# Performance work log

Hardware: AMD Instinct MI355X
Metric: run time of the kernel (lower is better)

The kernel has to match this reference:

```python
import jax, jax.numpy as jnp
import numpy as np

N_NODES = 50000
N_EDGES = 800000
HIDDEN = 128
MAX_Z = 1000
NUM_GRAPHS = 1000
NODES_PER_GRAPH = N_NODES // NUM_GRAPHS


def setup_inputs() -> dict:
    key = jax.random.key(0)
    ks = jax.random.split(key, 12)
    s = 1.0 / np.sqrt(HIDDEN)
    inp = {
        "z": jax.random.randint(ks[0], (N_NODES,), 0, MAX_Z),
        "edge_index": jax.random.randint(ks[1], (2, N_EDGES), 0, N_NODES),
        # sorted batch ids, 50 nodes per graph (SEAL-style subgraph batch)
        "batch": jnp.repeat(jnp.arange(NUM_GRAPHS), NODES_PER_GRAPH),
        "num_graphs": NUM_GRAPHS,
        "emb_table": jax.random.normal(ks[2], (MAX_Z, HIDDEN), jnp.float32),
        "w0": jax.random.normal(ks[3], (HIDDEN, HIDDEN), jnp.float32) * s,
        "b0": jnp.zeros((HIDDEN,), jnp.float32),
        "w1": jax.random.normal(ks[4], (HIDDEN, HIDDEN), jnp.float32) * s,
        "b1": jnp.zeros((HIDDEN,), jnp.float32),
        "w2": jax.random.normal(ks[5], (HIDDEN, HIDDEN), jnp.float32) * s,
        "b2": jnp.zeros((HIDDEN,), jnp.float32),
        "lin1_w": jax.random.normal(ks[6], (HIDDEN, HIDDEN), jnp.float32) * s,
        "lin1_b": jnp.zeros((HIDDEN,), jnp.float32),
        "lin2_w": jax.random.normal(ks[7], (HIDDEN, 1), jnp.float32) * s,
        "lin2_b": jnp.zeros((1,), jnp.float32),
    }
    return inp


def reference(z, edge_index, batch, num_graphs, emb_table, w0, b0, w1, b1, w2, b2,
              lin1_w, lin1_b, lin2_w, lin2_b):
    n = z.shape[0]
    # GCN symmetric normalization with self-loops (PyG gcn_norm, edge_weight=1)
    loops = jnp.arange(n)
    src = jnp.concatenate([edge_index[0], loops])
    dst = jnp.concatenate([edge_index[1], loops])
    ones = jnp.ones(src.shape[0], dtype=emb_table.dtype)
    deg = jax.ops.segment_sum(ones, dst, num_segments=n)
    dinv = jnp.where(deg > 0, jax.lax.rsqrt(deg), 0.0)
    norm = dinv[src] * dinv[dst]  # [E+N]

    def gcn_conv(x, W, b):
        h = x @ W  # linear transform first (bias added after aggregation)
        msg = h[src] * norm[:, None]  # gather + scale over edges
        return jax.ops.segment_sum(msg, dst, num_segments=n) + b

    x = emb_table[z]  # z embedding (z is 1-D -> no sum over dim 1)
    # dropout is identity in eval mode
    x = jax.nn.relu(gcn_conv(x, w0, b0))
    x = jax.nn.relu(gcn_conv(x, w1, b1))
    x = gcn_conv(x, w2, b2)

    # first occurrence of each batch id (batch is sorted per PyG convention)
    center = jax.ops.segment_min(jnp.arange(n), batch, num_segments=num_graphs)
    g = x[center] * x[center + 1]  # [G, H] pairwise link readout
    g = jax.nn.relu(g @ lin1_w + lin1_b)
    return g @ lin2_w + lin2_b  # [G, 1]
```

## Files before the change

### kernel.cpp

```cpp
#include <hip/hip_runtime.h>
#include <hip/hip_fp16.h>
#include <cstdint>
#include <cstddef>

#define H 128

typedef _Float16 f16x8 __attribute__((ext_vector_type(8)));
typedef float f32x4 __attribute__((ext_vector_type(4)));

__device__ inline float2 up2(unsigned u) {
    return __half22float2(*reinterpret_cast<const __half2*>(&u));
}
__device__ inline unsigned pk2(float a, float b) {
    __half2 h = __floats2half2_rn(a, b);
    return *reinterpret_cast<unsigned*>(&h);
}

__global__ void init_kernel(int* __restrict__ fill, int n,
                            const float* __restrict__ w0, const float* __restrict__ w1,
                            const float* __restrict__ w2, _Float16* __restrict__ wt) {
    int idx = blockIdx.x * 256 + threadIdx.x;
    if (idx < n) fill[idx] = 0;
    if (idx < 3 * H * H) {
        int m = idx >> 14;
        int c = (idx >> 7) & 127;
        int k = idx & 127;
        const float* W = (m == 0) ? w0 : (m == 1) ? w1 : w2;
        wt[idx] = (_Float16)W[k * H + c];
    }
}

__global__ __launch_bounds__(256) void fill_xcd(const int* __restrict__ src,
                                                const int* __restrict__ dst, int E,
                                                int* __restrict__ fill,
                                                unsigned short* __restrict__ csr_pad,
                                                int n, int rs) {
    int p = blockIdx.x & 7;
    int lo = p * rs;
    int hi = lo + rs; if (hi > n) hi = n;
    int nchunks = gridDim.x >> 3;
    int chunk = blockIdx.x >> 3;
    int stride = nchunks * 256;
    int E4 = E >> 2;
    const int4* dst4 = reinterpret_cast<const int4*>(dst);

    for (int q = chunk * 256 + threadIdx.x; q < E4; q += stride) {
        int4 d4 = dst4[q];
        int e = q * 4;
        if (d4.x >= lo && d4.x < hi) {
            int s = src[e];
            int pos = atomicAdd(&fill[d4.x], 1);
            if (pos < 64) csr_pad[(d4.x << 6) + pos] = (unsigned short)s;
        }
        if (d4.y >= lo && d4.y < hi) {
            int s = src[e + 1];
            int pos = atomicAdd(&fill[d4.y], 1);
            if (pos < 64) csr_pad[(d4.y << 6) + pos] = (unsigned short)s;
        }
        if (d4.z >= lo && d4.z < hi) {
            int s = src[e + 2];
            int pos = atomicAdd(&fill[d4.z], 1);
            if (pos < 64) csr_pad[(d4.z << 6) + pos] = (unsigned short)s;
        }
        if (d4.w >= lo && d4.w < hi) {
            int s = src[e + 3];
            int pos = atomicAdd(&fill[d4.w], 1);
            if (pos < 64) csr_pad[(d4.w << 6) + pos] = (unsigned short)s;
        }
    }
    if (blockIdx.x < 8) {
        int e = E4 * 4 + threadIdx.x;
        if (e < E) {
            int d = dst[e];
            if (d >= lo && d < hi) {
                int s = src[e];
                int pos = atomicAdd(&fill[d], 1);
                if (pos < 64) csr_pad[(d << 6) + pos] = (unsigned short)s;
            }
        }
    }
}

__global__ void post_fill(const int* __restrict__ fill, float* __restrict__ dinv,
                          const int* __restrict__ batch, int* __restrict__ sel, int n) {
    int i = blockIdx.x * 256 + threadIdx.x;
    if (i < n) {
        dinv[i] = rsqrtf((float)(fill[i] + 1));
        int b = batch[i];
        if (i == 0 || batch[i - 1] != b) {
            sel[2 * b] = i;
            sel[2 * b + 1] = (i + 1 < n) ? i + 1 : n - 1;
        }
    }
}


template<int MODE>
__global__ __launch_bounds__(256) void gemm_mfma(const void* __restrict__ Xv,
                                                 const int* __restrict__ z,
                                                 const _Float16* __restrict__ Wt,
                                                 unsigned* __restrict__ Yh, int n) {
    __shared__ _Float16 Wl[H * H];
    __shared__ _Float16 Cl[64 * H];
    int tid = threadIdx.x;

    {
        const uint4* src = reinterpret_cast<const uint4*>(Wt);
        #pragma unroll
        for (int it = 0; it < 8; ++it) {
            int idx = it * 256 + tid;
            int c = idx >> 4, s = idx & 15;
            unsigned boff = (unsigned)(c * 256 + s * 16) ^ ((unsigned)(c & 7) << 4);
            *reinterpret_cast<uint4*>(reinterpret_cast<char*>(Wl) + boff) = src[idx];
        }
    }

    int m0 = blockIdx.x * 64;
    int wid = tid >> 6, lane = tid & 63;
    int l15 = lane & 15, lhi = lane >> 4;
    int grow = m0 + wid * 16 + l15;
    bool rowok = grow < n;

    const float* xrow32 = nullptr;
    const _Float16* xrow16 = nullptr;
    if (MODE == 0) {
        const float* X = (const float*)Xv;
        int zr = rowok ? z[grow] : 0;
        xrow32 = X + (size_t)zr * H;
    } else {
        const _Float16* X = (const _Float16*)Xv;
        xrow16 = X + (size_t)(rowok ? grow : 0) * H;
    }

    unsigned braw[8];
    unsigned swz = (unsigned)(l15 & 7) << 4;
    #pragma unroll
    for (int ct = 0; ct < 8; ++ct) {
        int c = ct * 16 + l15;
        braw[ct] = (unsigned)(c * 256 + lhi * 16);
    }

    f32x4 acc[8];
    #pragma unroll
    for (int ct = 0; ct < 8; ++ct) acc[ct] = (f32x4){0.f, 0.f, 0.f, 0.f};

    __syncthreads();

    #pragma unroll
    for (int kb = 0; kb < 4; ++kb) {
        f16x8 a;
        if (MODE == 0) {
            const float* ap = xrow32 + kb * 32 + lhi * 8;
            float4 x0 = *reinterpret_cast<const float4*>(ap);
            float4 x1 = *reinterpret_cast<const float4*>(ap + 4);
            a[0] = (_Float16)x0.x; a[1] = (_Float16)x0.y;
            a[2] = (_Float16)x0.z; a[3] = (_Float16)x0.w;
            a[4] = (_Float16)x1.x; a[5] = (_Float16)x1.y;
            a[6] = (_Float16)x1.z; a[7] = (_Float16)x1.w;
        } else {
            a = *reinterpret_cast<const f16x8*>(xrow16 + kb * 32 + lhi * 8);
        }
        #pragma unroll
        for (int ct = 0; ct < 8; ++ct) {
            unsigned boff = (braw[ct] + (unsigned)(kb * 64)) ^ swz;
            f16x8 b = *reinterpret_cast<const f16x8*>(
                reinterpret_cast<const char*>(Wl) + boff);
            acc[ct] = __builtin_amdgcn_mfma_f32_16x16x32_f16(a, b, acc[ct], 0, 0, 0);
        }
    }

    _Float16* cw = Cl + wid * 16 * H;
    #pragma unroll
    for (int ct = 0; ct < 8; ++ct) {
        #pragma unroll
        for (int r = 0; r < 4; ++r) {
            int row = lhi * 4 + r;
            int col = ct * 16 + l15;
            cw[row * H + col] = (_Float16)acc[ct][r];
        }
    }
    int orow = lane >> 2, oseg = lane & 3;
    int growo = m0 + wid * 16 + orow;
    if (growo < n) {
        const uint4* cp = reinterpret_cast<const uint4*>(
            reinterpret_cast<const char*>(cw) + orow * 256 + oseg * 64);
        uint4* dp = reinterpret_cast<uint4*>(
            reinterpret_cast<char*>(Yh) + (size_t)growo * 256 + oseg * 64);
        dp[0] = cp[0]; dp[1] = cp[1]; dp[2] = cp[2]; dp[3] = cp[3];
    }
}


__device__ inline float4 agg_core(const unsigned* __restrict__ Hb,
                                  const unsigned short* __restrict__ csr_pad,
                                  const float* __restrict__ dinv,
                                  const float* __restrict__ bias,
                                  int node, int deg, float di,
                                  int lane, int half, int l32) {
    const uint2* Hu = reinterpret_cast<const uint2*>(Hb);
    float4 acc0 = make_float4(0.f, 0.f, 0.f, 0.f);
    float4 acc1 = make_float4(0.f, 0.f, 0.f, 0.f);
    float4 acc2 = make_float4(0.f, 0.f, 0.f, 0.f);
    float4 acc3 = make_float4(0.f, 0.f, 0.f, 0.f);
    if (half == 0) {
        float s = di * di;
        uint2 u = Hu[(size_t)node * 32 + l32];
        float4 bv = reinterpret_cast<const float4*>(bias)[l32];
        float2 f0 = up2(u.x), f1 = up2(u.y);
        acc0.x = bv.x + f0.x * s;
        acc0.y = bv.y + f0.y * s;
        acc0.z = bv.z + f1.x * s;
        acc0.w = bv.w + f1.y * s;
    }
    int beg = node << 6;
    int end = beg + deg;
    int j = beg + half;
    for (; j + 6 < end; j += 8) {
        int s0 = csr_pad[j];
        int s1 = csr_pad[j + 2];
        int s2 = csr_pad[j + 4];
        int s3 = csr_pad[j + 6];
        uint2 u0 = Hu[(size_t)s0 * 32 + l32];
        uint2 u1 = Hu[(size_t)s1 * 32 + l32];
        uint2 u2 = Hu[(size_t)s2 * 32 + l32];
        uint2 u3 = Hu[(size_t)s3 * 32 + l32];
        float n0 = dinv[s0] * di;
        float n1 = dinv[s1] * di;
        float n2 = dinv[s2] * di;
        float n3 = dinv[s3] * di;
        float2 a0 = up2(u0.x), b0 = up2(u0.y);
        float2 a1 = up2(u1.x), b1 = up2(u1.y);
        float2 a2 = up2(u2.x), b2 = up2(u2.y);
        float2 a3 = up2(u3.x), b3 = up2(u3.y);
        acc0.x = fmaf(a0.x, n0, acc0.x); acc0.y = fmaf(a0.y, n0, acc0.y);
        acc0.z = fmaf(b0.x, n0, acc0.z); acc0.w = fmaf(b0.y, n0, acc0.w);
        acc1.x = fmaf(a1.x, n1, acc1.x); acc1.y = fmaf(a1.y, n1, acc1.y);
        acc1.z = fmaf(b1.x, n1, acc1.z); acc1.w = fmaf(b1.y, n1, acc1.w);
        acc2.x = fmaf(a2.x, n2, acc2.x); acc2.y = fmaf(a2.y, n2, acc2.y);
        acc2.z = fmaf(b2.x, n2, acc2.z); acc2.w = fmaf(b2.y, n2, acc2.w);
        acc3.x = fmaf(a3.x, n3, acc3.x); acc3.y = fmaf(a3.y, n3, acc3.y);
        acc3.z = fmaf(b3.x, n3, acc3.z); acc3.w = fmaf(b3.y, n3, acc3.w);
    }
    for (; j < end; j += 2) {
        int s0 = csr_pad[j];
        uint2 u0 = Hu[(size_t)s0 * 32 + l32];
        float n0 = dinv[s0] * di;
        float2 a0 = up2(u0.x), b0 = up2(u0.y);
        acc0.x = fmaf(a0.x, n0, acc0.x); acc0.y = fmaf(a0.y, n0, acc0.y);
        acc0.z = fmaf(b0.x, n0, acc0.z); acc0.w = fmaf(b0.y, n0, acc0.w);
    }
    acc0.x += acc1.x + acc2.x + acc3.x;
    acc0.y += acc1.y + acc2.y + acc3.y;
    acc0.z += acc1.z + acc2.z + acc3.z;
    acc0.w += acc1.w + acc2.w + acc3.w;
    acc0.x += __shfl_xor(acc0.x, 32);
    acc0.y += __shfl_xor(acc0.y, 32);
    acc0.z += __shfl_xor(acc0.z, 32);
    acc0.w += __shfl_xor(acc0.w, 32);
    return acc0;
}

__global__ __launch_bounds__(256) void agg_f16(const unsigned* __restrict__ Hb,
                                               const int* __restrict__ degc,
                                               const unsigned short* __restrict__ csr_pad,
                                               const float* __restrict__ dinv,
                                               const float* __restrict__ bias,
                                               unsigned* __restrict__ Out, int n) {
    int node = blockIdx.x * 4 + (threadIdx.x >> 6);
    if (node >= n) return;
    int lane = threadIdx.x & 63;
    int half = lane >> 5, l32 = lane & 31;
    int deg = degc[node]; if (deg > 64) deg = 64;
    float di = dinv[node];
    float4 a = agg_core(Hb, csr_pad, dinv, bias, node, deg, di, lane, half, l32);
    if (half == 0) {
        a.x = fmaxf(a.x, 0.f); a.y = fmaxf(a.y, 0.f);
        a.z = fmaxf(a.z, 0.f); a.w = fmaxf(a.w, 0.f);
        uint2 pv; pv.x = pk2(a.x, a.y); pv.y = pk2(a.z, a.w);
        reinterpret_cast<uint2*>(Out)[(size_t)node * 32 + l32] = pv;
    }
}

__global__ __launch_bounds__(128) void readout_fused(const unsigned* __restrict__ Hb,
                                                     const int* __restrict__ degc,
                                                     const unsigned short* __restrict__ csr_pad,
                                                     const float* __restrict__ dinv,
                                                     const float* __restrict__ biasL2,
                                                     const int* __restrict__ sel,
                                                     const float* __restrict__ w1,
                                                     const float* __restrict__ b1,
                                                     const float* __restrict__ w2,
                                                     const float* __restrict__ b2o,
                                                     float* __restrict__ out) {
    __shared__ float o0[H], o1[H];
    __shared__ float gv[H];
    __shared__ float red[H];
    int g = blockIdx.x;
    int tid = threadIdx.x;
    int w = tid >> 6;
    int lane = tid & 63;
    int half = lane >> 5, l32 = lane & 31;

    int node = sel[2 * g + w];
    int deg = degc[node]; if (deg > 64) deg = 64;
    float di = dinv[node];
    float4 a = agg_core(Hb, csr_pad, dinv, biasL2, node, deg, di, lane, half, l32);
    float* ov = w ? o1 : o0;
    if (half == 0)
        *reinterpret_cast<float4*>(&ov[4 * l32]) = a;
    __syncthreads();

    int c = tid;
    gv[c] = o0[c] * o1[c];
    __syncthreads();
    float acc = b1[c];
    #pragma unroll 8
    for (int k = 0; k < H; ++k)
        acc = fmaf(gv[k], w1[k * H + c], acc);
    acc = fmaxf(acc, 0.f);
    red[c] = acc * w2[c];
    __syncthreads();
    for (int off = 64; off > 0; off >>= 1) {
        if (c < off) red[c] += red[c + off];
        __syncthreads();
    }
    if (c == 0) out[g] = red[0] + b2o[0];
}


static inline size_t align_up(size_t x) { return (x + 255) & ~(size_t)255; }

extern "C" void kernel_launch(void* const* d_in, const int* in_sizes, int n_in,
                              void* d_out, int out_size, void* d_ws, size_t ws_size,
                              hipStream_t stream) {
    const int n = in_sizes[0];
    const int E = in_sizes[1] / 2;
    const int G = out_size;

    const int*   z      = (const int*)d_in[0];
    const int*   ei     = (const int*)d_in[1];
    const int*   batch  = (const int*)d_in[2];
    const float* emb    = (const float*)d_in[4];
    const float* w0     = (const float*)d_in[5];
    const float* b0     = (const float*)d_in[6];
    const float* w1     = (const float*)d_in[7];
    const float* b1     = (const float*)d_in[8];
    const float* w2     = (const float*)d_in[9];
    const float* b2     = (const float*)d_in[10];
    const float* lin1_w = (const float*)d_in[11];
    const float* lin1_b = (const float*)d_in[12];
    const float* lin2_w = (const float*)d_in[13];
    const float* lin2_b = (const float*)d_in[14];

    const int* e_src = ei;
    const int* e_dst = ei + E;

    const int rs = (n + 7) / 8;

    char* p = (char*)d_ws;
    int*            fill     = (int*)p;            p += align_up((size_t)n * 4);
    int*            sel      = (int*)p;            p += align_up((size_t)2 * G * 4);
    unsigned short* csr_pad  = (unsigned short*)p; p += align_up((size_t)n * 64 * 2);
    float*          dinv     = (float*)p;          p += align_up((size_t)n * 4);
    _Float16*       wt       = (_Float16*)p;       p += align_up((size_t)3 * H * H * 2);
    unsigned*       hB       = (unsigned*)p;       p += align_up((size_t)n * 64 * 4);
    unsigned*       hA       = (unsigned*)p;       p += align_up((size_t)n * 64 * 4);

    const int TB = 256;
    dim3 gN((n + TB - 1) / TB);

    init_kernel<<<gN, TB, 0, stream>>>(fill, n, w0, w1, w2, wt);
    fill_xcd<<<2048, 256, 0, stream>>>(e_src, e_dst, E, fill, csr_pad, n, rs);
    post_fill<<<gN, TB, 0, stream>>>(fill, dinv, batch, sel, n);

    dim3 gemm_grid((n + 63) / 64);
    dim3 agg_grid((n + 3) / 4);

    gemm_mfma<0><<<gemm_grid, 256, 0, stream>>>(emb, z, wt, hB, n);
    agg_f16<<<agg_grid, 256, 0, stream>>>(hB, fill, csr_pad, dinv, b0, hA, n);
    gemm_mfma<1><<<gemm_grid, 256, 0, stream>>>(hA, nullptr, wt + H * H, hB, n);
    agg_f16<<<agg_grid, 256, 0, stream>>>(hB, fill, csr_pad, dinv, b1, hA, n);
    gemm_mfma<1><<<gemm_grid, 256, 0, stream>>>(hA, nullptr, wt + 2 * H * H, hB, n);
    readout_fused<<<G, 128, 0, stream>>>(hB, fill, csr_pad, dinv, b2, sel,
                                         lin1_w, lin1_b, lin2_w, lin2_b,
                                         (float*)d_out);
}
```

Baseline: 172.7 us.

## Fuse CSR fill and first GEMM into one launch, reuse LDS for output staging

The independent CSR-building fill pass and the embedding GEMM are merged into a single kernel whose blocks split by index: the first blocks run the GEMM and the rest run the fill, so the two can overlap and one launch is saved. The GEMM body now reuses the weight LDS buffer to stage its output after a barrier, which halves its shared memory and may raise occupancy. In exchange, the fused kernel carries the larger LDS footprint into the fill blocks, which can lower their occupancy, and there is an extra __syncthreads per GEMM block.

```diff
diff --git a/kernel.cpp b/kernel.cpp
--- a/kernel.cpp
+++ b/kernel.cpp
@@ -4,6 +4,7 @@
 #include <cstddef>
 
 #define H 128
+#define NFILLB 2048
 
 typedef _Float16 f16x8 __attribute__((ext_vector_type(8)));
 typedef float f32x4 __attribute__((ext_vector_type(4)));
@@ -30,21 +31,20 @@
     }
 }
 
-__global__ __launch_bounds__(256) void fill_xcd(const int* __restrict__ src,
-                                                const int* __restrict__ dst, int E,
-                                                int* __restrict__ fill,
-                                                unsigned short* __restrict__ csr_pad,
-                                                int n, int rs) {
-    int p = blockIdx.x & 7;
+__device__ inline void fill_body(const int* __restrict__ src, const int* __restrict__ dst,
+                                 int E, int* __restrict__ fill,
+                                 unsigned short* __restrict__ csr_pad,
+                                 int n, int rs, int bid) {
+    int p = bid & 7;
     int lo = p * rs;
     int hi = lo + rs; if (hi > n) hi = n;
-    int nchunks = gridDim.x >> 3;
-    int chunk = blockIdx.x >> 3;
+    int nchunks = NFILLB >> 3;
+    int chunk = bid >> 3;
     int stride = nchunks * 256;
     int E4 = E >> 2;
     const int4* dst4 = reinterpret_cast<const int4*>(dst);
 
-    for (int q = chunk * 256 + threadIdx.x; q < E4; q += stride) {
+    for (int q = chunk * 256 + (int)threadIdx.x; q < E4; q += stride) {
         int4 d4 = dst4[q];
         int e = q * 4;
         if (d4.x >= lo && d4.x < hi) {
@@ -68,8 +68,8 @@
             if (pos < 64) csr_pad[(d4.w << 6) + pos] = (unsigned short)s;
         }
     }
-    if (blockIdx.x < 8) {
-        int e = E4 * 4 + threadIdx.x;
+    if (bid < 8) {
+        int e = E4 * 4 + (int)threadIdx.x;
         if (e < E) {
             int d = dst[e];
             if (d >= lo && d < hi) {
@@ -81,29 +81,13 @@
     }
 }
 
-__global__ void post_fill(const int* __restrict__ fill, float* __restrict__ dinv,
-                          const int* __restrict__ batch, int* __restrict__ sel, int n) {
-    int i = blockIdx.x * 256 + threadIdx.x;
-    if (i < n) {
-        dinv[i] = rsqrtf((float)(fill[i] + 1));
-        int b = batch[i];
-        if (i == 0 || batch[i - 1] != b) {
-            sel[2 * b] = i;
-            sel[2 * b + 1] = (i + 1 < n) ? i + 1 : n - 1;
-        }
-    }
-}
-
 
 template<int MODE>
-__global__ __launch_bounds__(256) void gemm_mfma(const void* __restrict__ Xv,
-                                                 const int* __restrict__ z,
-                                                 const _Float16* __restrict__ Wt,
-                                                 unsigned* __restrict__ Yh, int n) {
-    __shared__ _Float16 Wl[H * H];
-    __shared__ _Float16 Cl[64 * H];
+__device__ inline void gemm_body(const void* __restrict__ Xv, const int* __restrict__ z,
+                                 const _Float16* __restrict__ Wt,
+                                 unsigned* __restrict__ Yh, int n, int bidx,
+                                 _Float16* Wl) {
     int tid = threadIdx.x;
-
     {
         const uint4* src = reinterpret_cast<const uint4*>(Wt);
         #pragma unroll
@@ -115,7 +99,7 @@
         }
     }
 
-    int m0 = blockIdx.x * 64;
+    int m0 = bidx * 64;
     int wid = tid >> 6, lane = tid & 63;
     int l15 = lane & 15, lhi = lane >> 4;
     int grow = m0 + wid * 16 + l15;
@@ -169,7 +153,9 @@
         }
     }
 
-    _Float16* cw = Cl + wid * 16 * H;
+    __syncthreads();
+
+    _Float16* cw = Wl + wid * 16 * H;
     #pragma unroll
     for (int ct = 0; ct < 8; ++ct) {
         #pragma unroll
@@ -187,6 +173,45 @@
         uint4* dp = reinterpret_cast<uint4*>(
             reinterpret_cast<char*>(Yh) + (size_t)growo * 256 + oseg * 64);
         dp[0] = cp[0]; dp[1] = cp[1]; dp[2] = cp[2]; dp[3] = cp[3];
+    }
+}
+
+template<int MODE>
+__global__ __launch_bounds__(256) void gemm_mfma(const void* __restrict__ Xv,
+                                                 const int* __restrict__ z,
+                                                 const _Float16* __restrict__ Wt,
+                                                 unsigned* __restrict__ Yh, int n) {
+    __shared__ _Float16 Wl[H * H];
+    gemm_body<MODE>(Xv, z, Wt, Yh, n, blockIdx.x, Wl);
+}
+
+__global__ __launch_bounds__(256) void fill_gemm0(const int* __restrict__ src,
+                                                  const int* __restrict__ dst, int E,
+                                                  int* __restrict__ fill,
+                                                  unsigned short* __restrict__ csr_pad,
+                                                  int n, int rs,
+                                                  const float* __restrict__ emb,
+                                                  const int* __restrict__ z,
+                                                  const _Float16* __restrict__ wt,
+                                                  unsigned* __restrict__ hB, int ngemm) {
+    __shared__ _Float16 Wl[H * H];
+    if ((int)blockIdx.x < ngemm) {
+        gemm_body<0>(emb, z, wt, hB, n, blockIdx.x, Wl);
+    } else {
+        fill_body(src, dst, E, fill, csr_pad, n, rs, blockIdx.x - ngemm);
+    }
+}
+
+__global__ void post_fill(const int* __restrict__ fill, float* __restrict__ dinv,
+                          const int* __restrict__ batch, int* __restrict__ sel, int n) {
+    int i = blockIdx.x * 256 + threadIdx.x;
+    if (i < n) {
+        dinv[i] = rsqrtf((float)(fill[i] + 1));
+        int b = batch[i];
+        if (i == 0 || batch[i - 1] != b) {
+            sel[2 * b] = i;
+            sel[2 * b + 1] = (i + 1 < n) ? i + 1 : n - 1;
+        }
     }
 }
 
@@ -368,15 +393,16 @@
 
     const int TB = 256;
     dim3 gN((n + TB - 1) / TB);
+    const int ngemm = (n + 63) / 64;
 
     init_kernel<<<gN, TB, 0, stream>>>(fill, n, w0, w1, w2, wt);
-    fill_xcd<<<2048, 256, 0, stream>>>(e_src, e_dst, E, fill, csr_pad, n, rs);
+    fill_gemm0<<<ngemm + NFILLB, TB, 0, stream>>>(e_src, e_dst, E, fill, csr_pad, n, rs,
+                                                  emb, z, wt, hB, ngemm);
     post_fill<<<gN, TB, 0, stream>>>(fill, dinv, batch, sel, n);
 
-    dim3 gemm_grid((n + 63) / 64);
+    dim3 gemm_grid(ngemm);
     dim3 agg_grid((n + 3) / 4);
 
-    gemm_mfma<0><<<gemm_grid, 256, 0, stream>>>(emb, z, wt, hB, n);
     agg_f16<<<agg_grid, 256, 0, stream>>>(hB, fill, csr_pad, dinv, b0, hA, n);
     gemm_mfma<1><<<gemm_grid, 256, 0, stream>>>(hA, nullptr, wt + H * H, hB, n);
     agg_f16<<<agg_grid, 256, 0, stream>>>(hB, fill, csr_pad, dinv, b1, hA, n);
```

Measured after the change: 163.3 us. -5.4%, faster.
